# Kernel tuning notes

Measured on AMD Instinct MI355X. Metric: run time of the kernel, lower is better.

The kernel has to match this reference:

```python
import jax, jax.numpy as jnp
import numpy as np

OFFSETS = (1, 2, 4, 8, 16, 64, 96, 192, 384, 512, 768, 1024)
J = 12
J_LARGE = 8  # offsets with index >= 4 use phase rotation


def _shift(x, d):
    """Return x shifted so out[..., n, :] = x[..., n-d, :]; zeros where n < d.
    Shift is along axis 2 (the sequence axis of [B,H,N,...])."""
    pad = [(0, 0)] * x.ndim
    pad[2] = (d, 0)
    return jnp.pad(x, pad)[:, :, : x.shape[2]]


def setup_inputs() -> dict:
    key = jax.random.key(0)
    ks = jax.random.split(key, 9)
    B, H, N, HD = 2, 16, 4096, 64
    f = jnp.float32
    q = jax.random.normal(ks[0], (B, H, N, HD), f)
    k = jax.random.normal(ks[1], (B, H, N, HD), f)
    v = jax.random.normal(ks[2], (B, H, N, HD), f)
    pb = jax.random.normal(ks[3], (J, H), f) * 0.1          # per-offset per-head score bias
    se = jax.random.normal(ks[4], (J, HD), f) * 0.1         # per-offset score embedding
    phase_base = jax.random.normal(ks[5], (J_LARGE, H, 2), f) * 0.1
    phase_gain = jax.random.normal(ks[6], (J_LARGE, H, 2), f) * 0.1
    y_pre = jax.random.normal(ks[7], (B, H, N, 2), f)       # query-side phase features
    z_pre = jax.random.normal(ks[8], (B, H, N, 2), f)       # key-side phase features
    return dict(q=q, k=k, v=v, pb=pb, se=se, phase_base=phase_base,
                phase_gain=phase_gain, y_pre=y_pre, z_pre=z_pre)


def reference(q, k, v, pb, se, phase_base, phase_gain, y_pre, z_pre):
    B, H, N, HD = q.shape
    sc = 1.0 / float(np.sqrt(HD))
    n_idx = jnp.arange(N)

    # --- scores over the J fixed causal offsets: s_i[n] = (q_n . (k_{n-d} + se_i)) * sc + pb[i,h]
    scores = []
    for i, d in enumerate(OFFSETS):
        ks_ = _shift(k, d)  # key at n - d
        s = (jnp.einsum('bhnd,bhnd->bhn', q, ks_)
             + jnp.einsum('bhnd,d->bhn', q, se[i])) * sc
        s = s + pb[i][None, :, None]
        valid = (n_idx >= d)[None, None, :]
        scores.append(jnp.where(valid, s, -jnp.inf))
    scores = jnp.stack(scores, axis=-1)  # [B,H,N,J]

    lse = jax.nn.logsumexp(scores, axis=-1)            # [B,H,N]
    safe_lse = jnp.where(jnp.isfinite(lse), lse, 0.0)  # rows with no valid offset -> alpha = 0
    alpha = jnp.exp(scores - safe_lse[..., None])      # [B,H,N,J]; -inf scores give exactly 0

    # --- weighted sum of (phase-rotated) values
    out = jnp.zeros_like(q)
    for i, d in enumerate(OFFSETS):
        vs = _shift(v, d)  # value at n - d: [B,H,N,HD]
        if i >= 4:
            pi = i - 4
            zs = _shift(z_pre, d)  # key-side phase features at n - d: [B,H,N,2]
            # theta_p = base[pi,h,p] + gain[pi,h,p] * y_pre[n,p] * z_pre[n-d,p]
            theta = (phase_base[pi][None, :, None, :]
                     + phase_gain[pi][None, :, None, :] * y_pre * zs)  # [B,H,N,2]
            c, s_ = jnp.cos(theta), jnp.sin(theta)
            v0, v1, v2, v3 = vs[..., 0], vs[..., 1], vs[..., 2], vs[..., 3]
            rot = jnp.stack([c[..., 0] * v0 - s_[..., 0] * v1,
                             s_[..., 0] * v0 + c[..., 0] * v1,
                             c[..., 1] * v2 - s_[..., 1] * v3,
                             s_[..., 1] * v2 + c[..., 1] * v3], axis=-1)
            vs = jnp.concatenate([rot, vs[..., 4:]], axis=-1)
        out = out + alpha[..., i:i + 1] * vs
    return out
```

## Files before the change

### kernel.cpp

```cpp
#include <hip/hip_runtime.h>


namespace {

constexpr int J   = 12;
constexpr int B_  = 2;
constexpr int H_  = 16;
constexpr int N_  = 4096;
constexpr int HD_ = 64;
constexpr int OFFS[J] = {1, 2, 4, 8, 16, 64, 96, 192, 384, 512, 768, 1024};

using f32x4 = __attribute__((ext_vector_type(4))) float;
using f32x2 = __attribute__((ext_vector_type(2))) float;

#define GLOAD4(dst, off, base)                                              \
    asm volatile("global_load_dwordx4 %0, %1, %2"                           \
                 : "=v"(dst) : "v"(off), "s"(base) : "memory")
#define GLOAD2(dst, off, base)                                              \
    asm volatile("global_load_dwordx2 %0, %1, %2"                           \
                 : "=v"(dst) : "v"(off), "s"(base) : "memory")

template <int CTRL>
__device__ __forceinline__ float dpp_add(float x) {
    int s = __builtin_amdgcn_update_dpp(0, __builtin_bit_cast(int, x),
                                        CTRL, 0xF, 0xF, false);
    return x + __builtin_bit_cast(float, s);
}

__global__ __launch_bounds__(256, 3) void dsqg_kernel(
    const float* __restrict__ q, const float* __restrict__ k,
    const float* __restrict__ v, const float* __restrict__ pb,
    const float* __restrict__ se, const float* __restrict__ phase_base,
    const float* __restrict__ phase_gain, const float* __restrict__ y_pre,
    const float* __restrict__ z_pre, float* __restrict__ out)
{
    __shared__ f32x4 seS[J * 16];

    const int raw = blockIdx.x;
    const int per = gridDim.x >> 3;
    const int wid = (raw & 7) * per + (raw >> 3);

    const int bh    = wid >> 8;
    const int chunk = wid & 255;
    const int h     = bh & (H_ - 1);

    const int tid  = threadIdx.x;
    const int lane = tid & 63;
    const int wave = tid >> 6;
    const int grp  = lane & 15;
    const int n    = chunk * 16 + wave * 4 + (lane >> 4);

    if (tid < J * 16) seS[tid] = ((const f32x4*)se)[tid];

    const size_t bhbytes = (size_t)bh * (N_ * HD_ * 4);
    const char* qb = (const char*)q + bhbytes;
    const char* kb = (const char*)k + bhbytes;
    const char* vb = (const char*)v + bhbytes;
    char*       ob = (char*)out + bhbytes;
    const char* yb = (const char*)y_pre + (size_t)bh * (N_ * 8);
    const char* zb = (const char*)z_pre + (size_t)bh * (N_ * 8);

    const uint32_t gb   = (uint32_t)grp << 4;
    const uint32_t rowb = ((uint32_t)n << 8) + gb;
    const uint32_t nb8  = (uint32_t)n << 3;

    bool ok[J];
    uint32_t offb[J];
#pragma unroll
    for (int i = 0; i < J; ++i) {
        ok[i]   = (n >= OFFS[i]);
        offb[i] = ok[i] ? (rowb - ((uint32_t)OFFS[i] << 8)) : gb;
    }
    uint32_t zo[8];
#pragma unroll
    for (int pi = 0; pi < 8; ++pi)
        zo[pi] = ok[pi + 4] ? (nb8 - ((uint32_t)OFFS[pi + 4] << 3)) : 0u;

    __syncthreads();

    f32x4 qr;
    GLOAD4(qr, rowb, qb);

    f32x4 kr[J];
#pragma unroll
    for (int i = 0; i < J; ++i) GLOAD4(kr[i], offb[i], kb);

    f32x4 vr[J];
#pragma unroll
    for (int i = 0; i < J; ++i) GLOAD4(vr[i], offb[i], vb);

    f32x2 yp;
    GLOAD2(yp, nb8, yb);
    f32x2 zr[8];
#pragma unroll
    for (int pi = 0; pi < 8; ++pi) GLOAD2(zr[pi], zo[pi], zb);

    asm volatile("s_waitcnt vmcnt(21)" ::: "memory");
    __builtin_amdgcn_sched_barrier(0);

    float p[J];
#pragma unroll
    for (int i = 0; i < J; ++i) {
        const f32x4 seg = seS[i * 16 + grp];
        float t = qr.x * (kr[i].x + seg.x);
        t = fmaf(qr.y, kr[i].y + seg.y, t);
        t = fmaf(qr.z, kr[i].z + seg.z, t);
        p[i] = fmaf(qr.w, kr[i].w + seg.w, t);
    }

#pragma unroll
    for (int i = 0; i < J; ++i) {
        p[i] = dpp_add<0xB1>(p[i]);
        p[i] = dpp_add<0x4E>(p[i]);
        p[i] = dpp_add<0x124>(p[i]);
        p[i] = dpp_add<0x128>(p[i]);
    }

    const float sc = 0.125f;
    float e[J];
    float sum = 0.f;
#pragma unroll
    for (int i = 0; i < J; ++i) {
        const float si = fmaf(p[i], sc, pb[i * H_ + h]);
        e[i] = ok[i] ? __expf(si) : 0.f;
        sum += e[i];
    }

    asm volatile("s_waitcnt vmcnt(0)" ::: "memory");
    __builtin_amdgcn_sched_barrier(0);

    if (grp == 0) {
#pragma unroll
        for (int pi = 0; pi < 8; ++pi) {
            const int i = pi + 4;
            const float b0 = phase_base[(pi * H_ + h) * 2 + 0];
            const float b1 = phase_base[(pi * H_ + h) * 2 + 1];
            const float g0 = phase_gain[(pi * H_ + h) * 2 + 0];
            const float g1 = phase_gain[(pi * H_ + h) * 2 + 1];
            const float th0 = fmaf(g0, yp.x * zr[pi].x, b0);
            const float th1 = fmaf(g1, yp.y * zr[pi].y, b1);
            const float c0 = __cosf(th0), s0 = __sinf(th0);
            const float c1 = __cosf(th1), s1 = __sinf(th1);
            const float v0 = vr[i].x, v1 = vr[i].y, v2 = vr[i].z, v3 = vr[i].w;
            vr[i].x = c0 * v0 - s0 * v1;
            vr[i].y = s0 * v0 + c0 * v1;
            vr[i].z = c1 * v2 - s1 * v3;
            vr[i].w = s1 * v2 + c1 * v3;
        }
    }

    float4 acc = make_float4(0.f, 0.f, 0.f, 0.f);
#pragma unroll
    for (int i = 0; i < J; ++i) {
        acc.x = fmaf(e[i], vr[i].x, acc.x);
        acc.y = fmaf(e[i], vr[i].y, acc.y);
        acc.z = fmaf(e[i], vr[i].z, acc.z);
        acc.w = fmaf(e[i], vr[i].w, acc.w);
    }

    float4 res;
    if (n >= 1) {
        const float inv = __builtin_amdgcn_rcpf(sum);
        res = make_float4(acc.x * inv, acc.y * inv, acc.z * inv, acc.w * inv);
    } else {
        res = make_float4(0.f, 0.f, 0.f, 0.f);
    }
    *(float4*)(ob + rowb) = res;
}

}

extern "C" void kernel_launch(void* const* d_in, const int* in_sizes, int n_in,
                              void* d_out, int out_size, void* d_ws, size_t ws_size,
                              hipStream_t stream) {
    const float* q          = (const float*)d_in[0];
    const float* k          = (const float*)d_in[1];
    const float* v          = (const float*)d_in[2];
    const float* pb         = (const float*)d_in[3];
    const float* se         = (const float*)d_in[4];
    const float* phase_base = (const float*)d_in[5];
    const float* phase_gain = (const float*)d_in[6];
    const float* y_pre      = (const float*)d_in[7];
    const float* z_pre      = (const float*)d_in[8];
    float* out              = (float*)d_out;

    const int positions = B_ * H_ * N_;
    const int blocks    = positions / 16;
    dsqg_kernel<<<blocks, 256, 0, stream>>>(q, k, v, pb, se, phase_base,
                                            phase_gain, y_pre, z_pre, out);
}
```

Before: 178.8 us.

## Distribute phase rotation across lanes and defer V loads past score compute

Spreads the 8 phase-rotated offsets across the 16 lanes of each row group. Each of lanes t8=0..7 loads its own z, phase_base, phase_gain and one extra V chunk, rotates it, weights it by its selected alpha, and the results are reduced to lane 0 with DPP. This removes the serialized 8-iteration sin/cos loop that ran only on grp==0 lanes. V loads are issued after the QK dot products to lower peak register pressure, and launch bounds are raised to 4 blocks per CU to increase occupancy. The cost is an extra redundant V load per lane, extra DPP reductions, and select logic.

```diff
diff --git a/kernel.cpp b/kernel.cpp
--- a/kernel.cpp
+++ b/kernel.cpp
@@ -27,7 +27,7 @@
     return x + __builtin_bit_cast(float, s);
 }
 
-__global__ __launch_bounds__(256, 3) void dsqg_kernel(
+__global__ __launch_bounds__(256, 4) void dsqg_kernel(
     const float* __restrict__ q, const float* __restrict__ k,
     const float* __restrict__ v, const float* __restrict__ pb,
     const float* __restrict__ se, const float* __restrict__ phase_base,
@@ -35,6 +35,7 @@
     const float* __restrict__ z_pre, float* __restrict__ out)
 {
     __shared__ f32x4 seS[J * 16];
+    __shared__ int   dtab[8];
 
     const int raw = blockIdx.x;
     const int per = gridDim.x >> 3;
@@ -51,14 +52,17 @@
     const int n    = chunk * 16 + wave * 4 + (lane >> 4);
 
     if (tid < J * 16) seS[tid] = ((const f32x4*)se)[tid];
+    if (tid < 8)      dtab[tid] = OFFS[tid + 4];
 
     const size_t bhbytes = (size_t)bh * (N_ * HD_ * 4);
-    const char* qb = (const char*)q + bhbytes;
-    const char* kb = (const char*)k + bhbytes;
-    const char* vb = (const char*)v + bhbytes;
-    char*       ob = (char*)out + bhbytes;
-    const char* yb = (const char*)y_pre + (size_t)bh * (N_ * 8);
-    const char* zb = (const char*)z_pre + (size_t)bh * (N_ * 8);
+    const char* qb  = (const char*)q + bhbytes;
+    const char* kb  = (const char*)k + bhbytes;
+    const char* vb  = (const char*)v + bhbytes;
+    char*       ob  = (char*)out + bhbytes;
+    const char* yb  = (const char*)y_pre + (size_t)bh * (N_ * 8);
+    const char* zb  = (const char*)z_pre + (size_t)bh * (N_ * 8);
+    const char* pbb = (const char*)phase_base;
+    const char* pgb = (const char*)phase_gain;
 
     const uint32_t gb   = (uint32_t)grp << 4;
     const uint32_t rowb = ((uint32_t)n << 8) + gb;
@@ -71,31 +75,27 @@
         ok[i]   = (n >= OFFS[i]);
         offb[i] = ok[i] ? (rowb - ((uint32_t)OFFS[i] << 8)) : gb;
     }
-    uint32_t zo[8];
-#pragma unroll
-    for (int pi = 0; pi < 8; ++pi)
-        zo[pi] = ok[pi + 4] ? (nb8 - ((uint32_t)OFFS[pi + 4] << 3)) : 0u;
 
     __syncthreads();
+
+    const int t8 = grp & 7;
+    const int dl = dtab[t8];
+    const bool okl = (n >= dl);
+    const uint32_t zol  = okl ? (uint32_t)(n - dl) << 3 : 0u;
+    const uint32_t vxol = okl ? (uint32_t)(n - dl) << 8 : 0u;
+    const uint32_t pofs = (uint32_t)(t8 * H_ + h) << 3;
 
     f32x4 qr;
     GLOAD4(qr, rowb, qb);
-
     f32x4 kr[J];
 #pragma unroll
     for (int i = 0; i < J; ++i) GLOAD4(kr[i], offb[i], kb);
-
-    f32x4 vr[J];
-#pragma unroll
-    for (int i = 0; i < J; ++i) GLOAD4(vr[i], offb[i], vb);
-
-    f32x2 yp;
-    GLOAD2(yp, nb8, yb);
-    f32x2 zr[8];
-#pragma unroll
-    for (int pi = 0; pi < 8; ++pi) GLOAD2(zr[pi], zo[pi], zb);
-
-    asm volatile("s_waitcnt vmcnt(21)" ::: "memory");
+    f32x2 yp;  GLOAD2(yp,  nb8,  yb);
+    f32x2 zl;  GLOAD2(zl,  zol,  zb);
+    f32x2 pbs; GLOAD2(pbs, pofs, pbb);
+    f32x2 pgn; GLOAD2(pgn, pofs, pgb);
+
+    asm volatile("s_waitcnt vmcnt(4)" ::: "memory");
     __builtin_amdgcn_sched_barrier(0);
 
     float p[J];
@@ -108,6 +108,14 @@
         p[i] = fmaf(qr.w, kr[i].w + seg.w, t);
     }
 
+    __builtin_amdgcn_sched_barrier(0);
+    f32x4 vr[J];
+#pragma unroll
+    for (int i = 0; i < J; ++i) GLOAD4(vr[i], offb[i], vb);
+    f32x4 vx;
+    GLOAD4(vx, vxol, vb);
+    __builtin_amdgcn_sched_barrier(0);
+
 #pragma unroll
     for (int i = 0; i < J; ++i) {
         p[i] = dpp_add<0xB1>(p[i]);
@@ -129,34 +137,55 @@
     asm volatile("s_waitcnt vmcnt(0)" ::: "memory");
     __builtin_amdgcn_sched_barrier(0);
 
-    if (grp == 0) {
-#pragma unroll
-        for (int pi = 0; pi < 8; ++pi) {
-            const int i = pi + 4;
-            const float b0 = phase_base[(pi * H_ + h) * 2 + 0];
-            const float b1 = phase_base[(pi * H_ + h) * 2 + 1];
-            const float g0 = phase_gain[(pi * H_ + h) * 2 + 0];
-            const float g1 = phase_gain[(pi * H_ + h) * 2 + 1];
-            const float th0 = fmaf(g0, yp.x * zr[pi].x, b0);
-            const float th1 = fmaf(g1, yp.y * zr[pi].y, b1);
-            const float c0 = __cosf(th0), s0 = __sinf(th0);
-            const float c1 = __cosf(th1), s1 = __sinf(th1);
-            const float v0 = vr[i].x, v1 = vr[i].y, v2 = vr[i].z, v3 = vr[i].w;
-            vr[i].x = c0 * v0 - s0 * v1;
-            vr[i].y = s0 * v0 + c0 * v1;
-            vr[i].z = c1 * v2 - s1 * v3;
-            vr[i].w = s1 * v2 + c1 * v3;
-        }
-    }
-
-    float4 acc = make_float4(0.f, 0.f, 0.f, 0.f);
-#pragma unroll
-    for (int i = 0; i < J; ++i) {
-        acc.x = fmaf(e[i], vr[i].x, acc.x);
-        acc.y = fmaf(e[i], vr[i].y, acc.y);
-        acc.z = fmaf(e[i], vr[i].z, acc.z);
-        acc.w = fmaf(e[i], vr[i].w, acc.w);
-    }
+    const float s01 = (t8 & 1) ? e[5]  : e[4];
+    const float s23 = (t8 & 1) ? e[7]  : e[6];
+    const float s45 = (t8 & 1) ? e[9]  : e[8];
+    const float s67 = (t8 & 1) ? e[11] : e[10];
+    const float sA  = (t8 & 2) ? s23 : s01;
+    const float sB  = (t8 & 2) ? s67 : s45;
+    const float esel = (t8 & 4) ? sB : sA;
+
+    const float th0 = fmaf(pgn.x, yp.x * zl.x, pbs.x);
+    const float th1 = fmaf(pgn.y, yp.y * zl.y, pbs.y);
+    const float c0 = __cosf(th0), s0 = __sinf(th0);
+    const float c1 = __cosf(th1), s1 = __sinf(th1);
+    f32x4 cx;
+    cx.x = esel * (c0 * vx.x - s0 * vx.y);
+    cx.y = esel * (s0 * vx.x + c0 * vx.y);
+    cx.z = esel * (c1 * vx.z - s1 * vx.w);
+    cx.w = esel * (s1 * vx.z + c1 * vx.w);
+
+#pragma unroll
+    for (int st = 0; st < 1; ++st) { }
+    cx.x = dpp_add<0xB1>(cx.x); cx.y = dpp_add<0xB1>(cx.y);
+    cx.z = dpp_add<0xB1>(cx.z); cx.w = dpp_add<0xB1>(cx.w);
+    cx.x = dpp_add<0x4E>(cx.x); cx.y = dpp_add<0x4E>(cx.y);
+    cx.z = dpp_add<0x4E>(cx.z); cx.w = dpp_add<0x4E>(cx.w);
+    cx.x = dpp_add<0x124>(cx.x); cx.y = dpp_add<0x124>(cx.y);
+    cx.z = dpp_add<0x124>(cx.z); cx.w = dpp_add<0x124>(cx.w);
+
+    float4 accl = make_float4(0.f, 0.f, 0.f, 0.f);
+#pragma unroll
+    for (int i = 0; i < 4; ++i) {
+        accl.x = fmaf(e[i], vr[i].x, accl.x);
+        accl.y = fmaf(e[i], vr[i].y, accl.y);
+        accl.z = fmaf(e[i], vr[i].z, accl.z);
+        accl.w = fmaf(e[i], vr[i].w, accl.w);
+    }
+    float4 acch = accl;
+#pragma unroll
+    for (int i = 4; i < J; ++i) {
+        acch.x = fmaf(e[i], vr[i].x, acch.x);
+        acch.y = fmaf(e[i], vr[i].y, acch.y);
+        acch.z = fmaf(e[i], vr[i].z, acch.z);
+        acch.w = fmaf(e[i], vr[i].w, acch.w);
+    }
+    const bool lo = (grp == 0);
+    float4 acc;
+    acc.x = lo ? accl.x + cx.x : acch.x;
+    acc.y = lo ? accl.y + cx.y : acch.y;
+    acc.z = lo ? accl.z + cx.z : acch.z;
+    acc.w = lo ? accl.w + cx.w : acch.w;
 
     float4 res;
     if (n >= 1) {
```

New measurement: 183.7 us. +2.7%, slower.

## Tile 64 positions per block with LDS window for short offsets and pipelined loads

Applied to the files above, without the earlier changes.

Each block now handles 64 consecutive positions instead of 16. It stages an 80-row window of K and V in LDS so the five short offsets (1 to 16) read from shared memory, while the long offsets are still fetched from global memory through a double-buffered prefetch across four iterations. The phase rotation is spread across the first 8 lanes of each 16-lane group, each lane doing one large offset, and the results are combined with DPP reductions. This is meant to cut redundant global traffic and raise memory-level parallelism, at the cost of LDS usage, more register pressure, and fewer blocks.

```diff
diff --git a/kernel.cpp b/kernel.cpp
--- a/kernel.cpp
+++ b/kernel.cpp
@@ -9,6 +9,8 @@
 constexpr int N_  = 4096;
 constexpr int HD_ = 64;
 constexpr int OFFS[J] = {1, 2, 4, 8, 16, 64, 96, 192, 384, 512, 768, 1024};
+constexpr int T_  = 64;
+constexpr int W_  = 80;
 
 using f32x4 = __attribute__((ext_vector_type(4))) float;
 using f32x2 = __attribute__((ext_vector_type(2))) float;
@@ -20,12 +22,151 @@
     asm volatile("global_load_dwordx2 %0, %1, %2"                           \
                  : "=v"(dst) : "v"(off), "s"(base) : "memory")
 
+#define VMWAIT(N)                                                           \
+    asm volatile("s_waitcnt vmcnt(" #N ")" ::: "memory");                   \
+    __builtin_amdgcn_sched_barrier(0)
+
 template <int CTRL>
 __device__ __forceinline__ float dpp_add(float x) {
     int s = __builtin_amdgcn_update_dpp(0, __builtin_bit_cast(int, x),
                                         CTRL, 0xF, 0xF, false);
     return x + __builtin_bit_cast(float, s);
 }
+
+#define ISSUEA(nn, QR, KR, YP, ZL) do {                                     \
+    const int nA_ = (nn);                                                   \
+    const uint32_t rbA_ = ((uint32_t)nA_ << 8) + gbl;                       \
+    GLOAD4(QR, rbA_, qb);                                                   \
+    _Pragma("unroll")                                                       \
+    for (int i = 5; i < J; ++i) {                                           \
+        const uint32_t oA_ = (nA_ >= OFFS[i])                               \
+            ? (rbA_ - ((uint32_t)OFFS[i] << 8)) : gbl;                      \
+        GLOAD4(KR[i - 5], oA_, kb);                                         \
+    }                                                                       \
+    const uint32_t nb8A_ = (uint32_t)nA_ << 3;                              \
+    GLOAD2(YP, nb8A_, yb);                                                  \
+    const uint32_t zoA_ = (nA_ >= dl) ? ((uint32_t)(nA_ - dl) << 3) : 0u;   \
+    GLOAD2(ZL, zoA_, zb);                                                   \
+} while (0)
+
+#define ITERBODY(NVAL, TOPN, TAILN, PREF, QR, KR, YP, ZL, QRN, KRN, YPN, ZLN) \
+do {                                                                        \
+    const int n_ = (NVAL);                                                  \
+    const uint32_t rowb_ = ((uint32_t)n_ << 8) + gbl;                       \
+    VMWAIT(TOPN);                                   \
+    const int rbase_ = n_ - P + 16;                        \
+    float p_[J];                                                            \
+    _Pragma("unroll")                                                       \
+    for (int i = 0; i < 5; ++i) {                                           \
+        const f32x4 kk  = kS[(rbase_ - OFFS[i]) * 16 + grp];                \
+        const f32x4 seg = seS[i * 16 + grp];                                \
+        float t = QR.x * (kk.x + seg.x);                                    \
+        t = fmaf(QR.y, kk.y + seg.y, t);                                    \
+        t = fmaf(QR.z, kk.z + seg.z, t);                                    \
+        p_[i] = fmaf(QR.w, kk.w + seg.w, t);                                \
+    }                                                                       \
+    _Pragma("unroll")                                                       \
+    for (int i = 5; i < J; ++i) {                                           \
+        const f32x4 kk  = KR[i - 5];                                        \
+        const f32x4 seg = seS[i * 16 + grp];                                \
+        float t = QR.x * (kk.x + seg.x);                                    \
+        t = fmaf(QR.y, kk.y + seg.y, t);                                    \
+        t = fmaf(QR.z, kk.z + seg.z, t);                                    \
+        p_[i] = fmaf(QR.w, kk.w + seg.w, t);                                \
+    }                                                                       \
+                  \
+    f32x4 vr_[7];                                                           \
+    _Pragma("unroll")                                                       \
+    for (int i = 5; i < J; ++i) {                                           \
+        const uint32_t oB_ = (n_ >= OFFS[i])                                \
+            ? (rowb_ - ((uint32_t)OFFS[i] << 8)) : gbl;                     \
+        GLOAD4(vr_[i - 5], oB_, vb);                                        \
+    }                                                                       \
+    f32x4 vx_;                                                              \
+    const uint32_t vxo_ = (n_ >= dl) ? ((uint32_t)(n_ - dl) << 8) : 0u;     \
+    GLOAD4(vx_, vxo_, vb);                                                  \
+    if (PREF) { ISSUEA(n_ + 4, QRN, KRN, YPN, ZLN); }                       \
+          \
+    _Pragma("unroll")                                                       \
+    for (int i = 0; i < J; ++i) {                                           \
+        p_[i] = dpp_add<0xB1>(p_[i]);      \
+        p_[i] = dpp_add<0x4E>(p_[i]);      \
+        p_[i] = dpp_add<0x124>(p_[i]);                       \
+        p_[i] = dpp_add<0x128>(p_[i]);                       \
+    }                                                                       \
+    float e_[J];                                                            \
+    float sum_ = 0.f;                                                       \
+    _Pragma("unroll")                                                       \
+    for (int i = 0; i < J; ++i) {                                           \
+        const float si = fmaf(p_[i], 0.125f, pbh[i]);                       \
+        e_[i] = (n_ >= OFFS[i]) ? __expf(si) : 0.f;                         \
+        sum_ += e_[i];                                                      \
+    }                                                                       \
+    VMWAIT(TAILN);                  \
+                \
+    const float s01_ = (t8 & 1) ? e_[5]  : e_[4];                           \
+    const float s23_ = (t8 & 1) ? e_[7]  : e_[6];                           \
+    const float s45_ = (t8 & 1) ? e_[9]  : e_[8];                           \
+    const float s67_ = (t8 & 1) ? e_[11] : e_[10];                          \
+    const float sA_  = (t8 & 2) ? s23_ : s01_;                              \
+    const float sB_  = (t8 & 2) ? s67_ : s45_;                              \
+    const float esel_ = (t8 & 4) ? sB_ : sA_;                               \
+    const float th0_ = fmaf(pgn.x, YP.x * ZL.x, pbs.x);                     \
+    const float th1_ = fmaf(pgn.y, YP.y * ZL.y, pbs.y);                     \
+    const float c0_ = __cosf(th0_), s0_ = __sinf(th0_);                     \
+    const float c1_ = __cosf(th1_), s1_ = __sinf(th1_);                     \
+    f32x4 cx_;                                                              \
+    cx_.x = esel_ * (c0_ * vx_.x - s0_ * vx_.y);                            \
+    cx_.y = esel_ * (s0_ * vx_.x + c0_ * vx_.y);                            \
+    cx_.z = esel_ * (c1_ * vx_.z - s1_ * vx_.w);                            \
+    cx_.w = esel_ * (s1_ * vx_.z + c1_ * vx_.w);                            \
+    cx_.x = dpp_add<0xB1>(cx_.x);  cx_.y = dpp_add<0xB1>(cx_.y);            \
+    cx_.z = dpp_add<0xB1>(cx_.z);  cx_.w = dpp_add<0xB1>(cx_.w);            \
+    cx_.x = dpp_add<0x4E>(cx_.x);  cx_.y = dpp_add<0x4E>(cx_.y);            \
+    cx_.z = dpp_add<0x4E>(cx_.z);  cx_.w = dpp_add<0x4E>(cx_.w);            \
+    cx_.x = dpp_add<0x124>(cx_.x); cx_.y = dpp_add<0x124>(cx_.y);           \
+    cx_.z = dpp_add<0x124>(cx_.z); cx_.w = dpp_add<0x124>(cx_.w);           \
+                     \
+    float4 accl_ = make_float4(0.f, 0.f, 0.f, 0.f);                         \
+    _Pragma("unroll")                                                       \
+    for (int i = 0; i < 4; ++i) {                                           \
+        const f32x4 vv = vS[(rbase_ - OFFS[i]) * 16 + grp];                 \
+        accl_.x = fmaf(e_[i], vv.x, accl_.x);                               \
+        accl_.y = fmaf(e_[i], vv.y, accl_.y);                               \
+        accl_.z = fmaf(e_[i], vv.z, accl_.z);                               \
+        accl_.w = fmaf(e_[i], vv.w, accl_.w);                               \
+    }                                                                       \
+    float4 acch_ = accl_;                                                   \
+    {                                                                       \
+        const f32x4 vv = vS[(rbase_ - 16) * 16 + grp];                      \
+        acch_.x = fmaf(e_[4], vv.x, acch_.x);                               \
+        acch_.y = fmaf(e_[4], vv.y, acch_.y);                               \
+        acch_.z = fmaf(e_[4], vv.z, acch_.z);                               \
+        acch_.w = fmaf(e_[4], vv.w, acch_.w);                               \
+    }                                                                       \
+    _Pragma("unroll")                                                       \
+    for (int i = 5; i < J; ++i) {                                           \
+        acch_.x = fmaf(e_[i], vr_[i - 5].x, acch_.x);                       \
+        acch_.y = fmaf(e_[i], vr_[i - 5].y, acch_.y);                       \
+        acch_.z = fmaf(e_[i], vr_[i - 5].z, acch_.z);                       \
+        acch_.w = fmaf(e_[i], vr_[i - 5].w, acch_.w);                       \
+    }                                                                       \
+    const bool lo_ = (grp == 0);                                            \
+    float4 acc_;                                                            \
+    acc_.x = lo_ ? accl_.x + cx_.x : acch_.x;                               \
+    acc_.y = lo_ ? accl_.y + cx_.y : acch_.y;                               \
+    acc_.z = lo_ ? accl_.z + cx_.z : acch_.z;                               \
+    acc_.w = lo_ ? accl_.w + cx_.w : acch_.w;                               \
+    float4 res_;                                                            \
+    if (n_ >= 1) {                                                          \
+        const float inv_ = __builtin_amdgcn_rcpf(sum_);                     \
+        res_ = make_float4(acc_.x * inv_, acc_.y * inv_,                    \
+                           acc_.z * inv_, acc_.w * inv_);                   \
+    } else {                                                                \
+        res_ = make_float4(0.f, 0.f, 0.f, 0.f);                             \
+    }                                                                       \
+    *(float4*)(ob + rowb_) = res_;        \
+} while (0)
 
 __global__ __launch_bounds__(256, 3) void dsqg_kernel(
     const float* __restrict__ q, const float* __restrict__ k,
@@ -34,21 +175,24 @@
     const float* __restrict__ phase_gain, const float* __restrict__ y_pre,
     const float* __restrict__ z_pre, float* __restrict__ out)
 {
+    __shared__ f32x4 kS[W_ * 16];
+    __shared__ f32x4 vS[W_ * 16];
     __shared__ f32x4 seS[J * 16];
 
     const int raw = blockIdx.x;
     const int per = gridDim.x >> 3;
     const int wid = (raw & 7) * per + (raw >> 3);
 
-    const int bh    = wid >> 8;
-    const int chunk = wid & 255;
-    const int h     = bh & (H_ - 1);
+    const int bh  = wid >> 6;
+    const int blk = wid & 63;
+    const int h   = bh & (H_ - 1);
+    const int P   = blk * T_;
 
     const int tid  = threadIdx.x;
     const int lane = tid & 63;
     const int wave = tid >> 6;
     const int grp  = lane & 15;
-    const int n    = chunk * 16 + wave * 4 + (lane >> 4);
+    const int sub  = lane >> 4;
 
     if (tid < J * 16) seS[tid] = ((const f32x4*)se)[tid];
 
@@ -60,112 +204,57 @@
     const char* yb = (const char*)y_pre + (size_t)bh * (N_ * 8);
     const char* zb = (const char*)z_pre + (size_t)bh * (N_ * 8);
 
-    const uint32_t gb   = (uint32_t)grp << 4;
-    const uint32_t rowb = ((uint32_t)n << 8) + gb;
-    const uint32_t nb8  = (uint32_t)n << 3;
-
-    bool ok[J];
-    uint32_t offb[J];
+    {
+        const int r0 = P - 16;
 #pragma unroll
-    for (int i = 0; i < J; ++i) {
-        ok[i]   = (n >= OFFS[i]);
-        offb[i] = ok[i] ? (rowb - ((uint32_t)OFFS[i] << 8)) : gb;
-    }
-    uint32_t zo[8];
-#pragma unroll
-    for (int pi = 0; pi < 8; ++pi)
-        zo[pi] = ok[pi + 4] ? (nb8 - ((uint32_t)OFFS[pi + 4] << 3)) : 0u;
-
-    __syncthreads();
-
-    f32x4 qr;
-    GLOAD4(qr, rowb, qb);
-
-    f32x4 kr[J];
-#pragma unroll
-    for (int i = 0; i < J; ++i) GLOAD4(kr[i], offb[i], kb);
-
-    f32x4 vr[J];
-#pragma unroll
-    for (int i = 0; i < J; ++i) GLOAD4(vr[i], offb[i], vb);
-
-    f32x2 yp;
-    GLOAD2(yp, nb8, yb);
-    f32x2 zr[8];
-#pragma unroll
-    for (int pi = 0; pi < 8; ++pi) GLOAD2(zr[pi], zo[pi], zb);
-
-    asm volatile("s_waitcnt vmcnt(21)" ::: "memory");
-    __builtin_amdgcn_sched_barrier(0);
-
-    float p[J];
-#pragma unroll
-    for (int i = 0; i < J; ++i) {
-        const f32x4 seg = seS[i * 16 + grp];
-        float t = qr.x * (kr[i].x + seg.x);
-        t = fmaf(qr.y, kr[i].y + seg.y, t);
-        t = fmaf(qr.z, kr[i].z + seg.z, t);
-        p[i] = fmaf(qr.w, kr[i].w + seg.w, t);
-    }
-
-#pragma unroll
-    for (int i = 0; i < J; ++i) {
-        p[i] = dpp_add<0xB1>(p[i]);
-        p[i] = dpp_add<0x4E>(p[i]);
-        p[i] = dpp_add<0x124>(p[i]);
-        p[i] = dpp_add<0x128>(p[i]);
-    }
-
-    const float sc = 0.125f;
-    float e[J];
-    float sum = 0.f;
-#pragma unroll
-    for (int i = 0; i < J; ++i) {
-        const float si = fmaf(p[i], sc, pb[i * H_ + h]);
-        e[i] = ok[i] ? __expf(si) : 0.f;
-        sum += e[i];
-    }
-
-    asm volatile("s_waitcnt vmcnt(0)" ::: "memory");
-    __builtin_amdgcn_sched_barrier(0);
-
-    if (grp == 0) {
-#pragma unroll
-        for (int pi = 0; pi < 8; ++pi) {
-            const int i = pi + 4;
-            const float b0 = phase_base[(pi * H_ + h) * 2 + 0];
-            const float b1 = phase_base[(pi * H_ + h) * 2 + 1];
-            const float g0 = phase_gain[(pi * H_ + h) * 2 + 0];
-            const float g1 = phase_gain[(pi * H_ + h) * 2 + 1];
-            const float th0 = fmaf(g0, yp.x * zr[pi].x, b0);
-            const float th1 = fmaf(g1, yp.y * zr[pi].y, b1);
-            const float c0 = __cosf(th0), s0 = __sinf(th0);
-            const float c1 = __cosf(th1), s1 = __sinf(th1);
-            const float v0 = vr[i].x, v1 = vr[i].y, v2 = vr[i].z, v3 = vr[i].w;
-            vr[i].x = c0 * v0 - s0 * v1;
-            vr[i].y = s0 * v0 + c0 * v1;
-            vr[i].z = c1 * v2 - s1 * v3;
-            vr[i].w = s1 * v2 + c1 * v3;
+        for (int t = 0; t < (W_ * 16) / 256; ++t) {
+            const int idx = t * 256 + tid;
+            const int row = idx >> 4;
+            const int col = idx & 15;
+            int gr = r0 + row;
+            gr = gr < 0 ? 0 : gr;
+            const uint32_t go = ((uint32_t)gr << 8) + ((uint32_t)col << 4);
+            kS[idx] = *(const f32x4*)(kb + go);
+            vS[idx] = *(const f32x4*)(vb + go);
         }
     }
 
-    float4 acc = make_float4(0.f, 0.f, 0.f, 0.f);
+    const int t8  = grp & 7;
+    const int d01 = (t8 & 1) ? 64   : 16;
+    const int d23 = (t8 & 1) ? 192  : 96;
+    const int d45 = (t8 & 1) ? 512  : 384;
+    const int d67 = (t8 & 1) ? 1024 : 768;
+    const int dA  = (t8 & 2) ? d23 : d01;
+    const int dB  = (t8 & 2) ? d67 : d45;
+    const int dl  = (t8 & 4) ? dB : dA;
+
+    const uint32_t pofs = (uint32_t)(t8 * H_ + h) << 3;
+    const f32x2 pbs = *(const f32x2*)((const char*)phase_base + pofs);
+    const f32x2 pgn = *(const f32x2*)((const char*)phase_gain + pofs);
+    float pbh[J];
 #pragma unroll
-    for (int i = 0; i < J; ++i) {
-        acc.x = fmaf(e[i], vr[i].x, acc.x);
-        acc.y = fmaf(e[i], vr[i].y, acc.y);
-        acc.z = fmaf(e[i], vr[i].z, acc.z);
-        acc.w = fmaf(e[i], vr[i].w, acc.w);
-    }
-
-    float4 res;
-    if (n >= 1) {
-        const float inv = __builtin_amdgcn_rcpf(sum);
-        res = make_float4(acc.x * inv, acc.y * inv, acc.z * inv, acc.w * inv);
-    } else {
-        res = make_float4(0.f, 0.f, 0.f, 0.f);
-    }
-    *(float4*)(ob + rowb) = res;
+    for (int i = 0; i < J; ++i) pbh[i] = pb[i * H_ + h];
+
+    asm volatile("" :: "v"(pbs.x), "v"(pbs.y), "v"(pgn.x), "v"(pgn.y));
+    asm volatile("" :: "v"(pbh[0]), "v"(pbh[1]), "v"(pbh[2]), "v"(pbh[3]),
+                       "v"(pbh[4]), "v"(pbh[5]), "v"(pbh[6]), "v"(pbh[7]),
+                       "v"(pbh[8]), "v"(pbh[9]), "v"(pbh[10]), "v"(pbh[11]));
+
+    __syncthreads();
+
+    const uint32_t gbl = (uint32_t)grp << 4;
+    const int n0 = P + wave * 16 + sub;
+
+    f32x4 qrA, qrB;
+    f32x4 krA[7], krB[7];
+    f32x2 ypA, ypB, zlA, zlB;
+
+    ISSUEA(n0, qrA, krA, ypA, zlA);
+
+    ITERBODY(n0,      2, 10, 1, qrA, krA, ypA, zlA, qrB, krB, ypB, zlB);
+    ITERBODY(n0 + 4,  3, 10, 1, qrB, krB, ypB, zlB, qrA, krA, ypA, zlA);
+    ITERBODY(n0 + 8,  3, 10, 1, qrA, krA, ypA, zlA, qrB, krB, ypB, zlB);
+    ITERBODY(n0 + 12, 3,  0, 0, qrB, krB, ypB, zlB, qrA, krA, ypA, zlA);
 }
 
 }
@@ -185,7 +274,7 @@
     float* out              = (float*)d_out;
 
     const int positions = B_ * H_ * N_;
-    const int blocks    = positions / 16;
+    const int blocks    = positions / T_;
     dsqg_kernel<<<blocks, 256, 0, stream>>>(q, k, v, pb, se, phase_base,
                                             phase_gain, y_pre, z_pre, out);
 }
```

Result: faster. 173.7 us (-2.8%).
